# Kernel tuning notes

Hardware: AMD Instinct MI355X
Metric: run time of the kernel (lower is better)

The kernel has to match this reference:

```python
import jax, jax.numpy as jnp
import numpy as np

N_A = 50000
N_B = 50000
E = 500000
IN_F = 128
GNN_F = 16
OUT_F = 16
H = 8


def setup_inputs() -> dict:
    key = jax.random.key(0)
    ks = jax.random.split(key, 16)
    f32 = jnp.float32
    rn = lambda k, shape: jax.random.normal(k, shape, f32) * 0.05
    return {
        "idx_a": jnp.arange(N_A, dtype=jnp.int32),
        "idx_b": jnp.arange(N_B, dtype=jnp.int32),
        "src_r0": jax.random.randint(ks[0], (E,), 0, N_A, jnp.int32),
        "dst_r0": jax.random.randint(ks[1], (E,), 0, N_B, jnp.int32),
        "src_r1": jax.random.randint(ks[2], (E,), 0, N_B, jnp.int32),
        "dst_r1": jax.random.randint(ks[3], (E,), 0, N_A, jnp.int32),
        "emb_a": rn(ks[4], (N_A, IN_F)),
        "emb_b": rn(ks[5], (N_B, IN_F)),
        "l1_Wv": rn(ks[6], (2, IN_F, H * GNN_F)),
        "l1_bv": jnp.zeros((2, H * GNN_F), f32),
        "l1_Wq": rn(ks[7], (2, H * GNN_F, H)),
        "l1_bq": jnp.zeros((2, H), f32),
        "l1_Wk": rn(ks[8], (2, H * GNN_F, H)),
        "l1_bk": jnp.zeros((2, H), f32),
        "l2_Wv": rn(ks[9], (2, GNN_F, H * OUT_F)),
        "l2_bv": jnp.zeros((2, H * OUT_F), f32),
        "l2_Wq": rn(ks[10], (2, H * OUT_F, H)),
        "l2_bq": jnp.zeros((2, H), f32),
        "l2_Wk": rn(ks[11], (2, H * OUT_F, H)),
        "l2_bk": jnp.zeros((2, H), f32),
    }


def _gat(x_src, x_dst, src, dst, Wv, bv, Wq, bq, Wk, bk, n_dst, n_feat):
    # linear_v on src and dst node features
    h_src = x_src @ Wv + bv            # [Ns, H*F]
    h_dst = x_dst @ Wv + bv            # [Nd, H*F]
    q = h_dst @ Wq + bq                # [Nd, H]
    k = h_src @ Wk + bk                # [Ns, H]
    # u_add_v score + leaky relu, per edge per head
    e = jax.nn.leaky_relu(k[src] + q[dst], negative_slope=0.2)  # [E, H]
    # edge softmax over incoming edges of each destination node
    m = jax.ops.segment_max(e, dst, num_segments=n_dst)         # [Nd, H]
    ex = jnp.exp(e - m[dst])
    denom = jax.ops.segment_sum(ex, dst, num_segments=n_dst)    # [Nd, H]
    attn = ex / denom[dst]                                      # [E, H]
    # u_mul_e + scatter-sum aggregate
    u = h_src.reshape(-1, H, n_feat)                             # [Ns, H, F]
    msg = u[src] * attn[:, :, None]                              # [E, H, F]
    v = jax.ops.segment_sum(msg, dst, num_segments=n_dst)       # [Nd, H, F]
    return v.mean(axis=1)                                        # [Nd, F]


def reference(idx_a, idx_b, src_r0, dst_r0, src_r1, dst_r1, emb_a, emb_b,
              l1_Wv, l1_bv, l1_Wq, l1_bq, l1_Wk, l1_bk,
              l2_Wv, l2_bv, l2_Wq, l2_bq, l2_Wk, l2_bk):
    # REmbedding lookup per node type
    x_a = emb_a[idx_a]
    x_b = emb_b[idx_b]
    # layer 1: relation r0 (a->b) and r1 (b->a); each dst type has exactly 1
    # incoming relation, so the HeteroGraphConv mean is a no-op (count=1)
    h_b = _gat(x_a, x_b, src_r0, dst_r0, l1_Wv[0], l1_bv[0], l1_Wq[0], l1_bq[0],
               l1_Wk[0], l1_bk[0], N_B, GNN_F)
    h_a = _gat(x_b, x_a, src_r1, dst_r1, l1_Wv[1], l1_bv[1], l1_Wq[1], l1_bq[1],
               l1_Wk[1], l1_bk[1], N_A, GNN_F)
    # activation: Dropout(0.5) is identity in eval mode, then ELU
    h_a = jax.nn.elu(h_a)
    h_b = jax.nn.elu(h_b)
    # layer 2
    o_b = _gat(h_a, h_b, src_r0, dst_r0, l2_Wv[0], l2_bv[0], l2_Wq[0], l2_bq[0],
               l2_Wk[0], l2_bk[0], N_B, OUT_F)
    o_a = _gat(h_b, h_a, src_r1, dst_r1, l2_Wv[1], l2_bv[1], l2_Wq[1], l2_bq[1],
               l2_Wk[1], l2_bk[1], N_A, OUT_F)
    return (o_a, o_b)
```

## Files before the change

### kernel.cpp

```cpp
#include <hip/hip_runtime.h>
#include <hip/hip_fp16.h>

#define N_NODES 50000
#define NEDGE   500000
#define HEADS   8
#define FEAT    16
#define HF      128
#define UST     64
#define XKST    32

typedef __attribute__((ext_vector_type(8))) _Float16 half8;
typedef __attribute__((ext_vector_type(4))) float floatx4;

__device__ __forceinline__ unsigned pkh2(float a, float b) {
  __half2 h = __floats2half2_rn(a, b);
  return *(unsigned*)&h;
}

__global__ __launch_bounds__(256)
void prep_wt2_kernel(const float* __restrict__ W, const float* __restrict__ wf,
                     __half* __restrict__ Wt2, float* __restrict__ bias16) {
  int side = blockIdx.x;
  const float* Wp  = W + (size_t)side * 16384;
  const float* wfk = wf + (size_t)(side == 0 ? 1 : 3) * 1040;
  const float* wfq = wf + (size_t)(side == 0 ? 2 : 0) * 1040;
  __half* o = Wt2 + (size_t)side * 144 * 128;
  for (int j = threadIdx.x; j < 144 * 128; j += 256) {
    int col = j >> 7, k = j & 127;
    float v = (col < 128) ? Wp[k * 128 + col]
            : (col < 136) ? wfk[k * 8 + (col - 128)]
                          : wfq[k * 8 + (col - 136)];
    o[j] = __float2half(v);
  }
  if (threadIdx.x < 16) {
    int c = threadIdx.x;
    bias16[side * 16 + c] = (c < 8) ? wfk[1024 + c] : wfq[1024 + (c - 8)];
  }
}

__global__ __launch_bounds__(256)
void gemm_mfma_kernel(const float* __restrict__ xa, const int* __restrict__ idxa,
                      const float* __restrict__ xb, const int* __restrict__ idxb,
                      const __half* __restrict__ Wt2, const float* __restrict__ bias,
                      const float* __restrict__ bias16,
                      float* __restrict__ ua, float* __restrict__ ub,
                      float* __restrict__ kb0, float* __restrict__ kb1,
                      float* __restrict__ qb1, float* __restrict__ qb0, int nrows) {
  const int side = blockIdx.y;
  const float* x  = side ? xb : xa;
  const int* idx  = side ? idxb : idxa;
  const __half* Wtp = Wt2 + (size_t)side * 144 * 128;
  const float* bp = bias + side * HF;
  const float* b8 = bias16 + side * 16;
  float* uout = side ? ub : ua;
  float* kout = side ? kb1 : kb0;
  float* qout = side ? qb0 : qb1;

  __shared__ __align__(16) unsigned short sm[26624];
  char* Asm = (char*)sm;
  char* Wsm = (char*)(sm + 8192);
  const int tid = threadIdx.x;
  const int w = tid >> 6, lane = tid & 63;
  const int row0 = blockIdx.x * 64;

  #pragma unroll
  for (int p = 0; p < 9; ++p) {
    int i = p * 256 + tid;
    int col = i >> 4, kp = i & 15;
    float4 v = *(const float4*)(Wtp + col * 128 + kp * 8);
    int dst = (col * 256 + kp * 16) ^ ((col & 7) << 4);
    *(float4*)(Wsm + dst) = v;
  }
  {
    int r = tid >> 2;
    int rr = row0 + r;
    int g = (rr < nrows) ? (idx ? idx[rr] : rr) : 0;
    const float* xp = x + (size_t)g * 128 + (tid & 3) * 8;
    #pragma unroll
    for (int p = 0; p < 4; ++p) {
      float4 v0 = *(const float4*)(xp + p * 32);
      float4 v1 = *(const float4*)(xp + p * 32 + 4);
      uint4 o;
      o.x = pkh2(v0.x, v0.y); o.y = pkh2(v0.z, v0.w);
      o.z = pkh2(v1.x, v1.y); o.w = pkh2(v1.z, v1.w);
      int k0 = (tid & 3) * 8 + p * 32;
      int dst = (r * 256 + k0 * 2) ^ ((r & 7) << 4);
      *(uint4*)(Asm + dst) = o;
    }
  }
  __syncthreads();

  floatx4 acc[9];
  #pragma unroll
  for (int t = 0; t < 8; ++t) {
    float b = bp[t * 16 + (lane & 15)];
    acc[t] = (floatx4){b, b, b, b};
  }
  {
    float b = b8[lane & 15];
    acc[8] = (floatx4){b, b, b, b};
  }

  const int lrow = lane & 15, lk = lane >> 4;
  #pragma unroll
  for (int kb = 0; kb < 4; ++kb) {
    int r = w * 16 + lrow;
    int abyte = (r * 256 + kb * 64 + lk * 16) ^ ((r & 7) << 4);
    half8 af = *(const half8*)(Asm + abyte);
    #pragma unroll
    for (int t = 0; t < 9; ++t) {
      int c = t * 16 + lrow;
      int bbyte = (c * 256 + kb * 64 + lk * 16) ^ ((c & 7) << 4);
      half8 bf = *(const half8*)(Wsm + bbyte);
      acc[t] = __builtin_amdgcn_mfma_f32_16x16x32_f16(af, bf, acc[t], 0, 0, 0);
    }
  }

  unsigned short* up = (unsigned short*)uout;
  #pragma unroll
  for (int j = 0; j < 4; ++j) {
    int rr = row0 + w * 16 + (lane >> 4) * 4 + j;
    if (rr < nrows) {
      #pragma unroll
      for (int t = 0; t < 8; ++t) {
        __half h = __float2half(acc[t][j]);
        up[(size_t)rr * 128 + t * 16 + (lane & 15)] = *(unsigned short*)&h;
      }
      int col = lane & 15;
      if (col < 8) kout[(size_t)rr * 8 + col] = acc[8][j];
      else         qout[(size_t)rr * 8 + (col - 8)] = acc[8][j];
    }
  }
}

__global__ __launch_bounds__(256)
void fold_kernel(const float* __restrict__ l1_Wv, const float* __restrict__ l1_bv,
                 const float* __restrict__ l1_Wq, const float* __restrict__ l1_bq,
                 const float* __restrict__ l1_Wk, const float* __restrict__ l1_bk,
                 const float* __restrict__ l2_Wv, const float* __restrict__ l2_bv,
                 const float* __restrict__ l2_Wq, const float* __restrict__ l2_bq,
                 const float* __restrict__ l2_Wk, const float* __restrict__ l2_bk,
                 float* __restrict__ outbuf) {
  int b = blockIdx.x;
  int layer = b >> 2, rel = (b >> 1) & 1, qk = b & 1;
  int Kx = (layer == 0) ? 128 : 16;
  const float* Wv = ((layer == 0) ? l1_Wv : l2_Wv) + (size_t)rel * Kx * HF;
  const float* bv = ((layer == 0) ? l1_bv : l2_bv) + rel * HF;
  const float* Wqk = ((layer == 0) ? (qk ? l1_Wk : l1_Wq) : (qk ? l2_Wk : l2_Wq)) + (size_t)rel * HF * 8;
  const float* bqk = ((layer == 0) ? (qk ? l1_bk : l1_bq) : (qk ? l2_bk : l2_bq)) + rel * 8;
  float* o = outbuf + (size_t)b * 1040;
  for (int t = threadIdx.x; t < Kx * 8; t += 256) {
    int row = t >> 3, c = t & 7;
    float acc = 0.f;
    for (int j = 0; j < HF; ++j) acc += Wv[row * HF + j] * Wqk[j * 8 + c];
    o[t] = acc;
  }
  for (int t = threadIdx.x; t < 8; t += 256) {
    float acc = bqk[t];
    for (int j = 0; j < HF; ++j) acc += bv[j] * Wqk[j * 8 + t];
    o[Kx * 8 + t] = acc;
  }
}

__global__ __launch_bounds__(256)
void qk16_kernel(__half* __restrict__ xk_a, __half* __restrict__ xk_b,
                 const float* __restrict__ WfkA, const float* __restrict__ WfqA,
                 const float* __restrict__ WfkB, const float* __restrict__ WfqB,
                 float* __restrict__ qA, float* __restrict__ qB, int n) {
  const int side = blockIdx.y;
  __half* xk = side ? xk_b : xk_a;
  const float* Wfk = side ? WfkB : WfkA;
  const float* Wfq = side ? WfqB : WfqA;
  float* qout = side ? qB : qA;
  __shared__ float Wk[136], Wq[136];
  const int tid = threadIdx.x;
  for (int i = tid; i < 136; i += 256) { Wk[i] = Wfk[i]; Wq[i] = Wfq[i]; }
  __syncthreads();
  int row = blockIdx.x * 32 + (tid >> 3), col = tid & 7;
  if (row >= n) return;
  const __half* xr = xk + (size_t)row * XKST;
  uint4 p0 = *(const uint4*)xr;
  uint4 p1 = *(const uint4*)(xr + 8);
  float xv[16];
  {
    unsigned pp[8] = {p0.x, p0.y, p0.z, p0.w, p1.x, p1.y, p1.z, p1.w};
    #pragma unroll
    for (int j = 0; j < 8; ++j) {
      float2 f = __half22float2(*(__half2*)&pp[j]);
      xv[j * 2] = f.x; xv[j * 2 + 1] = f.y;
    }
  }
  float ak = Wk[128 + col], aq = Wq[128 + col];
  #pragma unroll
  for (int j = 0; j < 16; ++j) {
    ak += xv[j] * Wk[j * 8 + col];
    aq += xv[j] * Wq[j * 8 + col];
  }
  xk[(size_t)row * XKST + 16 + col] = __float2half(ak);
  qout[row * 8 + col] = aq;
}

__global__ __launch_bounds__(256)
void hist2_kernel(const int* __restrict__ dst0, const int* __restrict__ dst1,
                  int* __restrict__ cnt) {
  int e = blockIdx.x * 256 + threadIdx.x;
  if (e < NEDGE) atomicAdd(&cnt[dst0[e]], 1);
  else if (e < 2 * NEDGE) atomicAdd(&cnt[N_NODES + dst1[e - NEDGE]], 1);
}

__global__ __launch_bounds__(256)
void scan_bsum_kernel(const int* __restrict__ cnt, int* __restrict__ bsum, int n) {
  __shared__ int s[256];
  int i = blockIdx.x * 256 + threadIdx.x;
  s[threadIdx.x] = (i < n) ? cnt[i] : 0;
  __syncthreads();
  for (int o = 128; o > 0; o >>= 1) {
    if (threadIdx.x < o) s[threadIdx.x] += s[threadIdx.x + o];
    __syncthreads();
  }
  if (threadIdx.x == 0) bsum[blockIdx.x] = s[0];
}

__global__ __launch_bounds__(512)
void scan_offsets_kernel(int* __restrict__ bsum, int nb) {
  __shared__ int s[512];
  int t = threadIdx.x;
  s[t] = (t < nb) ? bsum[t] : 0;
  __syncthreads();
  for (int o = 1; o < 512; o <<= 1) {
    int v = (t >= o) ? s[t - o] : 0;
    __syncthreads();
    s[t] += v;
    __syncthreads();
  }
  if (t < nb) bsum[t] = (t == 0) ? 0 : s[t - 1];
}

__global__ __launch_bounds__(256)
void scan_final_kernel(const int* __restrict__ cnt, const int* __restrict__ boff,
                       int* __restrict__ row_start, int n) {
  __shared__ int s[256];
  int t = threadIdx.x, i = blockIdx.x * 256 + t;
  int v = (i < n) ? cnt[i] : 0;
  s[t] = v;
  __syncthreads();
  for (int o = 1; o < 256; o <<= 1) {
    int w = (t >= o) ? s[t - o] : 0;
    __syncthreads();
    s[t] += w;
    __syncthreads();
  }
  if (i < n)  row_start[i] = boff[blockIdx.x] + s[t] - v;
  if (i == n - 1) row_start[n] = boff[blockIdx.x] + s[t];
}

__global__ __launch_bounds__(256)
void csr_scatter2_kernel(const int* __restrict__ s0, const int* __restrict__ d0,
                         const int* __restrict__ s1, const int* __restrict__ d1,
                         const int* __restrict__ rs, int* __restrict__ fill,
                         int* __restrict__ cs) {
  int e = blockIdx.x * 256 + threadIdx.x;
  if (e >= 2 * NEDGE) return;
  int rel = (e >= NEDGE);
  int ee = rel ? e - NEDGE : e;
  int d = rel ? d1[ee] : d0[ee];
  int s = rel ? s1[ee] : s0[ee];
  int key = rel * N_NODES + d;
  int pos = rs[key] + atomicAdd(&fill[key], 1);
  cs[pos] = s;
}

__global__ __launch_bounds__(256)
void node_agg2_kernel(const int* __restrict__ rs, const int* __restrict__ cs,
                      const float* __restrict__ u0, const float* __restrict__ u1,
                      const float* __restrict__ kb0, const float* __restrict__ kb1,
                      const float* __restrict__ qt0, const float* __restrict__ qt1,
                      __half* __restrict__ out0, __half* __restrict__ out1) {
  int grp  = (blockIdx.x * 256 + threadIdx.x) >> 5;
  int lane = threadIdx.x & 31;
  if (grp >= 2 * N_NODES) return;
  int rel = grp >= N_NODES;
  int node = grp - (rel ? N_NODES : 0);
  const float* ut = rel ? u1 : u0;
  const float* kb = rel ? kb1 : kb0;
  const float* qt = rel ? qt1 : qt0;
  __half* out     = rel ? out1 : out0;

  int e0 = rs[grp], e1 = rs[grp + 1];
  const int hd = lane >> 2;
  float qh = qt[node * 8 + hd];
  float den = 0.f;
  float4 acc = make_float4(0.f, 0.f, 0.f, 0.f);

  for (int e = e0; e < e1; e += 8) {
    int m = e1 - e;
    int s[8];
    #pragma unroll
    for (int j = 0; j < 8; ++j) s[j] = cs[e + (j < m ? j : m - 1)];
    uint2 uv[8]; float kv[8];
    #pragma unroll
    for (int j = 0; j < 8; ++j) {
      uv[j] = *(const uint2*)((const char*)(ut + (size_t)s[j] * UST) + lane * 8);
      kv[j] = kb[s[j] * 8 + hd];
    }
    #pragma unroll
    for (int j = 0; j < 8; ++j) {
      float sc = kv[j] + qh; sc = sc > 0.f ? sc : 0.2f * sc;
      float ex = (j < m) ? __expf(sc) : 0.f;
      den += ex;
      float2 f01 = __half22float2(*(__half2*)&uv[j].x);
      float2 f23 = __half22float2(*(__half2*)&uv[j].y);
      acc.x += ex * f01.x; acc.y += ex * f01.y;
      acc.z += ex * f23.x; acc.w += ex * f23.y;
    }
  }
  float inv = den > 0.f ? 1.f / den : 0.f;
  float4 r = make_float4(acc.x * inv, acc.y * inv, acc.z * inv, acc.w * inv);
  #pragma unroll
  for (int m2 = 4; m2 <= 16; m2 <<= 1) {
    r.x += __shfl_xor(r.x, m2); r.y += __shfl_xor(r.y, m2);
    r.z += __shfl_xor(r.z, m2); r.w += __shfl_xor(r.w, m2);
  }
  r.x *= 0.125f; r.y *= 0.125f; r.z *= 0.125f; r.w *= 0.125f;
  r.x = r.x > 0.f ? r.x : expm1f(r.x);
  r.y = r.y > 0.f ? r.y : expm1f(r.y);
  r.z = r.z > 0.f ? r.z : expm1f(r.z);
  r.w = r.w > 0.f ? r.w : expm1f(r.w);
  if (lane < 4) {
    uint2 o;
    o.x = pkh2(r.x, r.y); o.y = pkh2(r.z, r.w);
    *(uint2*)&out[(size_t)node * XKST + lane * 4] = o;
  }
}

__global__ __launch_bounds__(256)
void agg_l2z_kernel(const int* __restrict__ rs, const int* __restrict__ cs,
                    const __half* __restrict__ xk_a, const __half* __restrict__ xk_b,
                    const float* __restrict__ qt0, const float* __restrict__ qt1,
                    const float* __restrict__ Wv, const float* __restrict__ bv,
                    float* __restrict__ out) {
  const int rel = blockIdx.y;
  __shared__ float Wt_lds[128 * 16];
  __shared__ float z_lds[8][128];
  __shared__ float bvs[16];
  const int tid = threadIdx.x;
  for (int i = tid; i < 2048; i += 256) {
    int j = i >> 7, c = i & 127, h = c >> 4, o = c & 15;
    Wt_lds[(h * 16 + j) * 16 + o] = Wv[rel * 2048 + i];
  }
  if (tid < 16) {
    float s = 0.f;
    #pragma unroll
    for (int h = 0; h < 8; ++h) s += bv[rel * 128 + h * 16 + tid];
    bvs[tid] = s;
  }
  __syncthreads();

  int node = blockIdx.x * 8 + (tid >> 5);
  int lane = tid & 31;
  int gl   = tid >> 5;
  const __half* xk = rel ? xk_b : xk_a;
  const float* qt = rel ? qt1 : qt0;
  int grp = rel * N_NODES + node;

  int e0 = rs[grp], e1 = rs[grp + 1];
  const int h = lane >> 2, fg = lane & 3;
  float qh = qt[node * 8 + h];
  float den = 0.f;
  float4 z = make_float4(0.f, 0.f, 0.f, 0.f);

  for (int e = e0; e < e1; e += 8) {
    int m = e1 - e;
    int s[8];
    #pragma unroll
    for (int j = 0; j < 8; ++j) s[j] = cs[e + (j < m ? j : m - 1)];
    uint2 uv[8]; __half kvh[8];
    #pragma unroll
    for (int j = 0; j < 8; ++j) {
      const __half* p = xk + (size_t)s[j] * XKST;
      uv[j] = *(const uint2*)(p + fg * 4);
      kvh[j] = p[16 + h];
    }
    #pragma unroll
    for (int j = 0; j < 8; ++j) {
      float sc = __half2float(kvh[j]) + qh; sc = sc > 0.f ? sc : 0.2f * sc;
      float ex = (j < m) ? __expf(sc) : 0.f;
      den += ex;
      float2 f01 = __half22float2(*(__half2*)&uv[j].x);
      float2 f23 = __half22float2(*(__half2*)&uv[j].y);
      z.x += ex * f01.x; z.y += ex * f01.y;
      z.z += ex * f23.x; z.w += ex * f23.y;
    }
  }
  float inv = den > 0.f ? 1.f / den : 0.f;
  z.x *= inv; z.y *= inv; z.z *= inv; z.w *= inv;
  *(float4*)&z_lds[gl][h * 16 + fg * 4] = z;

  const int o = lane & 15, half = lane >> 4;
  float acc = 0.f;
  #pragma unroll
  for (int hg = 0; hg < 4; ++hg) {
    int h2 = half * 4 + hg;
    const float* zr = &z_lds[gl][h2 * 16];
    float4 z0 = *(const float4*)zr;
    float4 z1 = *(const float4*)(zr + 4);
    float4 z2 = *(const float4*)(zr + 8);
    float4 z3 = *(const float4*)(zr + 12);
    const float* wb = &Wt_lds[h2 * 256 + o];
    acc += z0.x * wb[0]   + z0.y * wb[16]  + z0.z * wb[32]  + z0.w * wb[48]
         + z1.x * wb[64]  + z1.y * wb[80]  + z1.z * wb[96]  + z1.w * wb[112]
         + z2.x * wb[128] + z2.y * wb[144] + z2.z * wb[160] + z2.w * wb[176]
         + z3.x * wb[192] + z3.y * wb[208] + z3.z * wb[224] + z3.w * wb[240];
  }
  acc += __shfl_xor(acc, 16);
  if (lane < 16) {
    float r = 0.125f * (acc + ((e1 > e0) ? bvs[o] : 0.f));
    float* ob = out + (rel ? 0 : (size_t)N_NODES * FEAT);
    ob[(size_t)node * FEAT + o] = r;
  }
}

extern "C" void kernel_launch(void* const* d_in, const int* in_sizes, int n_in,
                              void* d_out, int out_size, void* d_ws, size_t ws_size,
                              hipStream_t stream) {
  const int* idx_a  = (const int*)d_in[0];
  const int* idx_b  = (const int*)d_in[1];
  const int* src_r0 = (const int*)d_in[2];
  const int* dst_r0 = (const int*)d_in[3];
  const int* src_r1 = (const int*)d_in[4];
  const int* dst_r1 = (const int*)d_in[5];
  const float* emb_a = (const float*)d_in[6];
  const float* emb_b = (const float*)d_in[7];
  const float* l1_Wv = (const float*)d_in[8];
  const float* l1_bv = (const float*)d_in[9];
  const float* l1_Wq = (const float*)d_in[10];
  const float* l1_bq = (const float*)d_in[11];
  const float* l1_Wk = (const float*)d_in[12];
  const float* l1_bk = (const float*)d_in[13];
  const float* l2_Wv = (const float*)d_in[14];
  const float* l2_bv = (const float*)d_in[15];
  const float* l2_Wq = (const float*)d_in[16];
  const float* l2_bq = (const float*)d_in[17];
  const float* l2_Wk = (const float*)d_in[18];
  const float* l2_bk = (const float*)d_in[19];
  float* out = (float*)d_out;

  char* ws = (char*)d_ws;
  size_t off = 0;
  auto alloc = [&](size_t bytes) {
    void* p = ws + off; off += (bytes + 255) & ~255ULL; return p;
  };
  float*  u0    = (float*)alloc((size_t)N_NODES * UST * 4);
  float*  u1    = (float*)alloc((size_t)N_NODES * UST * 4);
  __half* Wt2   = (__half*)alloc(2 * 144 * 128 * 2);
  float*  b16   = (float*)alloc(2 * 16 * 4);
  float*  kb0   = (float*)alloc((size_t)N_NODES * HEADS * 4);
  float*  kb1   = (float*)alloc((size_t)N_NODES * HEADS * 4);
  float*  qb0   = (float*)alloc((size_t)N_NODES * HEADS * 4);
  float*  qb1   = (float*)alloc((size_t)N_NODES * HEADS * 4);
  __half* xk_a  = (__half*)alloc((size_t)N_NODES * XKST * 2);
  __half* xk_b  = (__half*)alloc((size_t)N_NODES * XKST * 2);
  int*    rs    = (int*)  alloc((size_t)(2 * N_NODES + 1) * 4);
  int*    cs    = (int*)  alloc((size_t)2 * NEDGE * 4);
  int*    cnt   = (int*)  alloc((size_t)4 * N_NODES * 4);
  int*    bsum  = (int*)  alloc(512 * 4);
  float*  wf    = (float*)alloc(8 * 1040 * 4);

  dim3 blk(256);
  const int n2 = 2 * N_NODES;
  int* fill = cnt + n2;
  const int nScanBlk  = (n2 + 255) / 256;
  const int nEdgeBlk2 = (2 * NEDGE + 255) / 256;
  const int nAggBlk   = (n2 + 7) / 8;
  const int nAggL2    = N_NODES / 8;
  const int nGemmBlk64 = (N_NODES + 63) / 64;
  const int nQk16Blk   = (N_NODES + 31) / 32;

  fold_kernel<<<8, blk, 0, stream>>>(l1_Wv, l1_bv, l1_Wq, l1_bq, l1_Wk, l1_bk,
                                     l2_Wv, l2_bv, l2_Wq, l2_bq, l2_Wk, l2_bk, wf);
  prep_wt2_kernel<<<2, blk, 0, stream>>>(l1_Wv, wf, Wt2, b16);
  auto wslot = [&](int layer, int rel, int qk) {
    return wf + (size_t)((layer << 2) | (rel << 1) | qk) * 1040;
  };

  hipMemsetAsync(cnt, 0, (size_t)2 * n2 * 4, stream);
  hist2_kernel<<<nEdgeBlk2, blk, 0, stream>>>(dst_r0, dst_r1, cnt);
  scan_bsum_kernel<<<nScanBlk, blk, 0, stream>>>(cnt, bsum, n2);
  scan_offsets_kernel<<<1, dim3(512), 0, stream>>>(bsum, nScanBlk);
  scan_final_kernel<<<nScanBlk, blk, 0, stream>>>(cnt, bsum, rs, n2);
  csr_scatter2_kernel<<<nEdgeBlk2, blk, 0, stream>>>(src_r0, dst_r0, src_r1, dst_r1,
                                                     rs, fill, cs);

  {
    gemm_mfma_kernel<<<dim3(nGemmBlk64, 2), blk, 0, stream>>>(
        emb_a, idx_a, emb_b, idx_b, Wt2, l1_bv, b16,
        u0, u1, kb0, kb1, qb1, qb0, N_NODES);
    node_agg2_kernel<<<nAggBlk, blk, 0, stream>>>(rs, cs, u0, u1, kb0, kb1,
                                                  qb0, qb1, xk_b, xk_a);
  }
  {
    qk16_kernel<<<dim3(nQk16Blk, 2), blk, 0, stream>>>(
        xk_a, xk_b,
        wslot(1,0,1), wslot(1,1,0), wslot(1,1,1), wslot(1,0,0),
        qb1, qb0, N_NODES);
    agg_l2z_kernel<<<dim3(nAggL2, 2), blk, 0, stream>>>(
        rs, cs, xk_a, xk_b, qb0, qb1, l2_Wv, l2_bv, out);
  }
}
```

Before: 265.6 us.

## Sort destination nodes by in-degree to balance warps in aggregation kernels

Adds a counting-sort of destination nodes by in-degree (histogram, serial scan, scatter into a permutation). Both aggregation kernels read the node id from this permutation, so the eight 32-lane groups in a block handle nodes of similar degree. This targets divergence and load imbalance from random degrees. It costs three extra small kernel launches plus a memset, and makes node reads and output writes scattered instead of sequential.

```diff
diff --git a/kernel.cpp b/kernel.cpp
--- a/kernel.cpp
+++ b/kernel.cpp
@@ -271,16 +271,49 @@
 }
 
 __global__ __launch_bounds__(256)
+void dhist_kernel(const int* __restrict__ cnt, int* __restrict__ dcnt) {
+  int i = blockIdx.x * 256 + threadIdx.x;
+  if (i >= 2 * N_NODES) return;
+  int rel = i >= N_NODES;
+  int deg = cnt[i];
+  int b = deg > 31 ? 0 : 31 - deg;
+  atomicAdd(&dcnt[rel * 32 + b], 1);
+}
+
+__global__ void dscan_kernel(int* __restrict__ dcnt) {
+  if (threadIdx.x == 0 && blockIdx.x == 0) {
+    int a0 = 0, a1 = 0;
+    for (int b = 0; b < 32; ++b) { int c = dcnt[b];      dcnt[b] = a0;      a0 += c; }
+    for (int b = 0; b < 32; ++b) { int c = dcnt[32 + b]; dcnt[32 + b] = a1; a1 += c; }
+  }
+}
+
+__global__ __launch_bounds__(256)
+void dscatter_kernel(const int* __restrict__ cnt, int* __restrict__ doff,
+                     int* __restrict__ perm) {
+  int i = blockIdx.x * 256 + threadIdx.x;
+  if (i >= 2 * N_NODES) return;
+  int rel = i >= N_NODES;
+  int node = i - rel * N_NODES;
+  int deg = cnt[i];
+  int b = deg > 31 ? 0 : 31 - deg;
+  int pos = atomicAdd(&doff[rel * 32 + b], 1);
+  perm[rel * N_NODES + pos] = node;
+}
+
+__global__ __launch_bounds__(256)
 void node_agg2_kernel(const int* __restrict__ rs, const int* __restrict__ cs,
+                      const int* __restrict__ perm,
                       const float* __restrict__ u0, const float* __restrict__ u1,
                       const float* __restrict__ kb0, const float* __restrict__ kb1,
                       const float* __restrict__ qt0, const float* __restrict__ qt1,
                       __half* __restrict__ out0, __half* __restrict__ out1) {
-  int grp  = (blockIdx.x * 256 + threadIdx.x) >> 5;
+  int i    = (blockIdx.x * 256 + threadIdx.x) >> 5;
   int lane = threadIdx.x & 31;
-  if (grp >= 2 * N_NODES) return;
-  int rel = grp >= N_NODES;
-  int node = grp - (rel ? N_NODES : 0);
+  if (i >= 2 * N_NODES) return;
+  int rel = i >= N_NODES;
+  int node = perm[i];
+  int grp = rel * N_NODES + node;
   const float* ut = rel ? u1 : u0;
   const float* kb = rel ? kb1 : kb0;
   const float* qt = rel ? qt1 : qt0;
@@ -335,6 +368,7 @@
 
 __global__ __launch_bounds__(256)
 void agg_l2z_kernel(const int* __restrict__ rs, const int* __restrict__ cs,
+                    const int* __restrict__ perm,
                     const __half* __restrict__ xk_a, const __half* __restrict__ xk_b,
                     const float* __restrict__ qt0, const float* __restrict__ qt1,
                     const float* __restrict__ Wv, const float* __restrict__ bv,
@@ -356,9 +390,10 @@
   }
   __syncthreads();
 
-  int node = blockIdx.x * 8 + (tid >> 5);
+  int pos  = blockIdx.x * 8 + (tid >> 5);
   int lane = tid & 31;
   int gl   = tid >> 5;
+  int node = perm[rel * N_NODES + pos];
   const __half* xk = rel ? xk_b : xk_a;
   const float* qt = rel ? qt1 : qt0;
   int grp = rel * N_NODES + node;
@@ -463,6 +498,8 @@
   int*    rs    = (int*)  alloc((size_t)(2 * N_NODES + 1) * 4);
   int*    cs    = (int*)  alloc((size_t)2 * NEDGE * 4);
   int*    cnt   = (int*)  alloc((size_t)4 * N_NODES * 4);
+  int*    perm  = (int*)  alloc((size_t)2 * N_NODES * 4);
+  int*    dcnt  = (int*)  alloc(64 * 4);
   int*    bsum  = (int*)  alloc(512 * 4);
   float*  wf    = (float*)alloc(8 * 1040 * 4);
 
@@ -475,6 +512,7 @@
   const int nAggL2    = N_NODES / 8;
   const int nGemmBlk64 = (N_NODES + 63) / 64;
   const int nQk16Blk   = (N_NODES + 31) / 32;
+  const int nNodeBlk2  = (n2 + 255) / 256;
 
   fold_kernel<<<8, blk, 0, stream>>>(l1_Wv, l1_bv, l1_Wq, l1_bq, l1_Wk, l1_bk,
                                      l2_Wv, l2_bv, l2_Wq, l2_bq, l2_Wk, l2_bk, wf);
@@ -484,18 +522,22 @@
   };
 
   hipMemsetAsync(cnt, 0, (size_t)2 * n2 * 4, stream);
+  hipMemsetAsync(dcnt, 0, 64 * 4, stream);
   hist2_kernel<<<nEdgeBlk2, blk, 0, stream>>>(dst_r0, dst_r1, cnt);
   scan_bsum_kernel<<<nScanBlk, blk, 0, stream>>>(cnt, bsum, n2);
   scan_offsets_kernel<<<1, dim3(512), 0, stream>>>(bsum, nScanBlk);
   scan_final_kernel<<<nScanBlk, blk, 0, stream>>>(cnt, bsum, rs, n2);
   csr_scatter2_kernel<<<nEdgeBlk2, blk, 0, stream>>>(src_r0, dst_r0, src_r1, dst_r1,
                                                      rs, fill, cs);
+  dhist_kernel<<<nNodeBlk2, blk, 0, stream>>>(cnt, dcnt);
+  dscan_kernel<<<1, 64, 0, stream>>>(dcnt);
+  dscatter_kernel<<<nNodeBlk2, blk, 0, stream>>>(cnt, dcnt, perm);
 
   {
     gemm_mfma_kernel<<<dim3(nGemmBlk64, 2), blk, 0, stream>>>(
         emb_a, idx_a, emb_b, idx_b, Wt2, l1_bv, b16,
         u0, u1, kb0, kb1, qb1, qb0, N_NODES);
-    node_agg2_kernel<<<nAggBlk, blk, 0, stream>>>(rs, cs, u0, u1, kb0, kb1,
+    node_agg2_kernel<<<nAggBlk, blk, 0, stream>>>(rs, cs, perm, u0, u1, kb0, kb1,
                                                   qb0, qb1, xk_b, xk_a);
   }
   {
@@ -504,6 +546,6 @@
         wslot(1,0,1), wslot(1,1,0), wslot(1,1,1), wslot(1,0,0),
         qb1, qb0, N_NODES);
     agg_l2z_kernel<<<dim3(nAggL2, 2), blk, 0, stream>>>(
-        rs, cs, xk_a, xk_b, qb0, qb1, l2_Wv, l2_bv, out);
-  }
-}
+        rs, cs, perm, xk_a, xk_b, qb0, qb1, l2_Wv, l2_bv, out);
+  }
+}
```

New measurement: 759.2 us. 2.86x slower.
